# Optimization experiments

Hardware: AMD Instinct MI355X
Metric: run time of the kernel (lower is better)

The kernel has to match this reference:

```python
import jax, jax.numpy as jnp
import numpy as np

WINDOW = 256   # init kwarg window_size
CAUSAL = False # init kwarg causal


def setup_inputs() -> dict:
    key = jax.random.key(0)
    k1, k2, k3 = jax.random.split(key, 3)
    shape = (2, 16, 4096, 64)  # (batch, heads, seq_len, head_dim); seq_len % WINDOW == 0
    return {
        "query": jax.random.normal(k1, shape, dtype=jnp.float32),
        "key": jax.random.normal(k2, shape, dtype=jnp.float32),
        "value": jax.random.normal(k3, shape, dtype=jnp.float32),
    }


def _neighbor_blocks(x, nb, W):
    # x: [B,H,S,D] -> [B,H,nb,3W,D] where block n holds key blocks n-1,n,n+1 (zero padded at ends)
    B, H, S, D = x.shape
    xb = x.reshape(B, H, nb, W, D)
    xp = jnp.pad(xb, ((0, 0), (0, 0), (1, 1), (0, 0), (0, 0)))
    return jnp.concatenate([xp[:, :, j:j + nb] for j in range(3)], axis=3)


def _swa(query, key, value, window, causal):
    B, H, S, D = query.shape
    W = window
    nb = S // W
    scale = jnp.float32(1.0 / np.sqrt(D))
    qb = query.reshape(B, H, nb, W, D)
    kb = _neighbor_blocks(key, nb, W)    # [B,H,nb,3W,D]
    vb = _neighbor_blocks(value, nb, W)  # [B,H,nb,3W,D]

    # band mask: query global pos qi = n*W + q, key global pos ki = n*W + (k - W)
    qpos = jnp.arange(W)[:, None]              # [W,1]
    kpos = jnp.arange(3 * W)[None, :] - W      # [1,3W] relative block offset
    diff = kpos - qpos                         # [W,3W] == ki - qi
    ki = jnp.arange(nb)[:, None, None] * W + kpos[None]  # [nb,1,3W]
    valid = (ki >= 0) & (ki < S)
    if causal:
        band = (diff >= -W) & (diff <= 0)
    else:
        band = jnp.abs(diff) <= W
    mask = valid & band[None]                  # [nb,W,3W]

    scores = jnp.einsum('bhnqd,bhnkd->bhnqk', qb, kb) * scale  # [B,H,nb,W,3W]
    scores = jnp.where(mask, scores, -jnp.inf)
    attn = jax.nn.softmax(scores, axis=-1)
    out = jnp.einsum('bhnqk,bhnkd->bhnqd', attn, vb)
    return out.reshape(B, H, S, D)


def reference(query, key, value):
    return _swa(query, key, value, WINDOW, CAUSAL)
```

## Files before the change

### kernel.cpp

```cpp
#include <hip/hip_runtime.h>
#include <hip/hip_bf16.h>

typedef __attribute__((ext_vector_type(4)))  float f32x4;
typedef __attribute__((ext_vector_type(16))) float f32x16;
typedef __attribute__((ext_vector_type(8)))  short bf16x8;
typedef __attribute__((ext_vector_type(4)))  unsigned u32x4;

#define S_LEN 4096
#define HEAD_D 64
#define WIN 256
#define QBLK 128
#define KVBLK 64
#define KSTR 72
#define VSTR 72
#define QSCALE 0.18033688f

#define KBYTES (KVBLK * KSTR * 2)
#define VBYTES (HEAD_D * VSTR * 2)
#define KHALF  (KBYTES / 2)
#define VHALF  (VBYTES / 2)
#define LPAR_OFF (2 * KBYTES + 2 * VBYTES)
#define SMEM_BYTES (LPAR_OFF + 2 * 4 * 32 * 4)

static __device__ __forceinline__ unsigned cvt2(float lo, float hi) {
  unsigned r;
  asm("v_cvt_pk_bf16_f32 %0, %1, %2" : "=v"(r) : "v"(lo), "v"(hi));
  return r;
}

#define PUB_BARRIER() do {                              \
    __builtin_amdgcn_sched_barrier(0);                  \
    asm volatile("s_waitcnt lgkmcnt(0)" ::: "memory");  \
    __builtin_amdgcn_s_barrier();                       \
    __builtin_amdgcn_sched_barrier(0);                  \
  } while (0)

__global__ __launch_bounds__(512, 4)
void swa_fwd(const float* __restrict__ Q, const float* __restrict__ K,
             const float* __restrict__ V, float* __restrict__ O) {
  __shared__ __attribute__((aligned(16))) char smem[SMEM_BYTES];

  const int tid  = threadIdx.x;
  const int widx = tid >> 6;
  const int lane = tid & 63;
  const int hi   = lane >> 5;
  const int c    = lane & 31;
  const int qg   = widx & 3;
  const int kh   = widx >> 2;
  const int kho  = kh * 32;

  const int pb  = blockIdx.x;
  const int bh  = (pb & 7) * 4 + ((pb >> 3) >> 5);
  const int qb  = (pb >> 3) & 31;
  const int bq0 = qb * QBLK;
  const int q0w = bq0 + qg * 32;

  const size_t base = (size_t)bh * S_LEN * HEAD_D;
  const float* Qp = Q + base;
  const float* Kp = K + base;
  const float* Vp = V + base;
  float*       Op = O + base;

  const f32x16 Z16 = {0.f,0.f,0.f,0.f,0.f,0.f,0.f,0.f,0.f,0.f,0.f,0.f,0.f,0.f,0.f,0.f};

  bf16x8 aq[4];
  {
    const float* qr = Qp + (size_t)(q0w + c) * HEAD_D + hi * 8;
    #pragma unroll
    for (int ch = 0; ch < 4; ++ch) {
      f32x4 x0 = *(const f32x4*)(qr + ch * 16);
      f32x4 x1 = *(const f32x4*)(qr + ch * 16 + 4);
      u32x4 au;
      au[0] = cvt2(x0[0] * QSCALE, x0[1] * QSCALE);
      au[1] = cvt2(x0[2] * QSCALE, x0[3] * QSCALE);
      au[2] = cvt2(x1[0] * QSCALE, x1[1] * QSCALE);
      au[3] = cvt2(x1[2] * QSCALE, x1[3] * QSCALE);
      aq[ch] = __builtin_bit_cast(bf16x8, au);
    }
  }

  f32x16 acc0 = Z16, acc1 = Z16;
  float lsA = 0.f, lsB = 0.f;

  const int lo   = max(0, bq0 - WIN);
  const int khiB = min(S_LEN, bq0 + QBLK + WIN);
  const int nt   = (khiB - lo) >> 6;

  const int krow  = tid >> 3;
  const int kc8   = (tid & 7) << 3;
  const int key2  = (tid & 31) << 1;
  const int key2p = (key2 & ~12) | ((key2 & 4) << 1) | ((key2 & 8) >> 1);
  const int vd4   = (tid >> 5) << 2;

  short* const ksh = (short*)smem;
  short* const vsh = (short*)(smem + 2 * KBYTES);
  const short* const krd = ksh + (kho + c) * KSTR + hi * 8;
  const short* const vrd = vsh + c * VSTR + kho + hi * 8;
  short* const kwr = ksh + krow * KSTR + kc8;
  short* const vwr = vsh + vd4 * VSTR + key2p;

  unsigned koff = (unsigned)(lo + krow) * HEAD_D + kc8;
  unsigned voff = (unsigned)(lo + key2) * HEAD_D + vd4;

  f32x4 ka0, ka1, va0, va1;
  #define LOAD_TILE() do {                          \
    ka0 = *(const f32x4*)(Kp + koff);               \
    ka1 = *(const f32x4*)(Kp + koff + 4);           \
    va0 = *(const f32x4*)(Vp + voff);               \
    va1 = *(const f32x4*)(Vp + voff + HEAD_D);      \
    koff += KVBLK * HEAD_D;                         \
    voff += KVBLK * HEAD_D;                         \
  } while (0)

  #define STAGE_TO(BUF) do {                                        \
    u32x4 kw;                                                       \
    kw[0] = cvt2(ka0[0], ka0[1]);                                   \
    kw[1] = cvt2(ka0[2], ka0[3]);                                   \
    kw[2] = cvt2(ka1[0], ka1[1]);                                   \
    kw[3] = cvt2(ka1[2], ka1[3]);                                   \
    *(u32x4*)&kwr[(BUF) * KHALF] = kw;                              \
    _Pragma("unroll")                                               \
    for (int j = 0; j < 4; ++j)                                     \
      *(unsigned*)&vwr[(BUF) * VHALF + j * VSTR] = cvt2(va0[j], va1[j]); \
  } while (0)

  #define TILE_BODY(T, BUF) do {                                              \
    const int kv0_ = lo + ((T) << 6);                                         \
    f32x16 s = Z16;                                                           \
    __builtin_amdgcn_s_setprio(1);                                            \
    _Pragma("unroll")                                                         \
    for (int ch = 0; ch < 4; ++ch) {                                          \
      bf16x8 akf = *(const bf16x8*)&krd[(BUF) * KHALF + ch * 16];             \
      s = __builtin_amdgcn_mfma_f32_32x32x16_bf16(akf, aq[ch], s, 0, 0, 0);   \
    }                                                                         \
    __builtin_amdgcn_s_setprio(0);                                            \
    if ((T) + 1 < nt) {                                                       \
      STAGE_TO((BUF) ^ 1);                                                    \
      if ((T) + 2 < nt) LOAD_TILE();                                          \
    }                                                                         \
    const int rel_ = kv0_ + kho - q0w;                                        \
    if (rel_ >= -224 && rel_ <= 224) {                                        \
      _Pragma("unroll")                                                       \
      for (int g = 0; g < 16; g += 2) {                                       \
        const float p0 = __builtin_amdgcn_exp2f(s[g]);                        \
        const float p1 = __builtin_amdgcn_exp2f(s[g + 1]);                    \
        s[g] = p0; s[g + 1] = p1; lsA += p0; lsB += p1;                       \
      }                                                                       \
    } else {                                                                  \
      const int bm_ = rel_ + 4 * hi - c + WIN;                                \
      _Pragma("unroll")                                                       \
      for (int g = 0; g < 16; ++g) {                                          \
        const int ro_ = (g & 3) + 8 * (g >> 2);                               \
        const float p = ((unsigned)(bm_ + ro_) <= 2u * WIN)                   \
                          ? __builtin_amdgcn_exp2f(s[g]) : 0.f;               \
        s[g] = p; if (g & 1) lsB += p; else lsA += p;                         \
      }                                                                       \
    }                                                                         \
    __builtin_amdgcn_s_setprio(1);                                            \
    _Pragma("unroll")                                                         \
    for (int kt = 0; kt < 2; ++kt) {                                          \
      u32x4 pau;                                                              \
      _Pragma("unroll")                                                       \
      for (int p2 = 0; p2 < 4; ++p2)                                          \
        pau[p2] = cvt2(s[kt * 8 + 2 * p2], s[kt * 8 + 2 * p2 + 1]);           \
      const bf16x8 pa = __builtin_bit_cast(bf16x8, pau);                      \
      bf16x8 bv0 = *(const bf16x8*)&vrd[(BUF) * VHALF + kt * 16];             \
      acc0 = __builtin_amdgcn_mfma_f32_32x32x16_bf16(pa, bv0, acc0, 0, 0, 0); \
      bf16x8 bv1 = *(const bf16x8*)&vrd[(BUF) * VHALF + kt * 16 + 32 * VSTR]; \
      acc1 = __builtin_amdgcn_mfma_f32_32x32x16_bf16(pa, bv1, acc1, 0, 0, 0); \
    }                                                                         \
    __builtin_amdgcn_s_setprio(0);                                            \
    if ((T) + 1 < nt) PUB_BARRIER();                                          \
  } while (0)

  LOAD_TILE();
  STAGE_TO(0);
  LOAD_TILE();
  PUB_BARRIER();

  for (int t = 0; t < nt; t += 2) {
    TILE_BODY(t, 0);
    TILE_BODY(t + 1, 1);
  }

  float lsum = lsA + lsB;
  lsum += __shfl_xor(lsum, 32);
  __syncthreads();
  float* o_mrg = (float*)smem;
  float* l_par = (float*)(smem + LPAR_OFF);
  if (hi == 0) l_par[(kh * 4 + qg) * 32 + c] = lsum;
  if (kh == 0) {
    #pragma unroll
    for (int g = 0; g < 16; ++g) {
      const int qrow = (g & 3) + 8 * (g >> 2) + 4 * hi;
      o_mrg[(qg * 32 + qrow) * HEAD_D + c]      = acc0[g];
      o_mrg[(qg * 32 + qrow) * HEAD_D + 32 + c] = acc1[g];
    }
  }
  __syncthreads();
  if (kh == 1) {
    if (hi == 0) l_par[qg * 32 + c] = 1.0f / (l_par[qg * 32 + c] + l_par[(4 + qg) * 32 + c]);
    __asm__ volatile("s_waitcnt lgkmcnt(0)" ::: "memory");
    __builtin_amdgcn_sched_barrier(0);
    #pragma unroll
    for (int g = 0; g < 16; ++g) {
      const int qrow = (g & 3) + 8 * (g >> 2) + 4 * hi;
      const float iv = l_par[qg * 32 + qrow];
      float* orow = Op + (size_t)(q0w + qrow) * HEAD_D;
      orow[c]      = (o_mrg[(qg * 32 + qrow) * HEAD_D + c]      + acc0[g]) * iv;
      orow[32 + c] = (o_mrg[(qg * 32 + qrow) * HEAD_D + 32 + c] + acc1[g]) * iv;
    }
  }
}

extern "C" void kernel_launch(void* const* d_in, const int* in_sizes, int n_in,
                              void* d_out, int out_size, void* d_ws, size_t ws_size,
                              hipStream_t stream) {
  const float* q = (const float*)d_in[0];
  const float* k = (const float*)d_in[1];
  const float* v = (const float*)d_in[2];
  float* o = (float*)d_out;
  const int blocks = 2 * 16 * (S_LEN / QBLK);
  swa_fwd<<<dim3(blocks), dim3(512), 0, stream>>>(q, k, v, o);
}
```

Baseline: 47.22 us.

## Process KV tiles in pairs with four-buffer LDS and one barrier per pair

Restructures the main loop so each period computes QK^T for two 64-key tiles at once, from four LDS buffers (two pairs, ping-ponged). This halves the barriers and interleaves two independent MFMA chains. Staging of the next pair is spread between the softmax/PV phases. LDS use doubles (now dynamic shared memory with a per-launch attribute call) and launch bounds drop to 2 blocks per CU, which cuts occupancy and raises register pressure from holding two score tiles.

```diff
diff --git a/kernel.cpp b/kernel.cpp
--- a/kernel.cpp
+++ b/kernel.cpp
@@ -16,11 +16,10 @@
 #define QSCALE 0.18033688f
 
 #define KBYTES (KVBLK * KSTR * 2)
-#define VBYTES (HEAD_D * VSTR * 2)
-#define KHALF  (KBYTES / 2)
-#define VHALF  (VBYTES / 2)
-#define LPAR_OFF (2 * KBYTES + 2 * VBYTES)
-#define SMEM_BYTES (LPAR_OFF + 2 * 4 * 32 * 4)
+#define KELEM  (KVBLK * KSTR)
+#define VELEM  (HEAD_D * VSTR)
+#define LPAR_OFF (8 * KBYTES)
+#define SMEM_TOTAL (LPAR_OFF + 2 * 4 * 32 * 4)
 
 static __device__ __forceinline__ unsigned cvt2(float lo, float hi) {
   unsigned r;
@@ -35,10 +34,10 @@
     __builtin_amdgcn_sched_barrier(0);                  \
   } while (0)
 
-__global__ __launch_bounds__(512, 4)
+__global__ __launch_bounds__(512, 2)
 void swa_fwd(const float* __restrict__ Q, const float* __restrict__ K,
              const float* __restrict__ V, float* __restrict__ O) {
-  __shared__ __attribute__((aligned(16))) char smem[SMEM_BYTES];
+  extern __shared__ __align__(16) char smem[];
 
   const int tid  = threadIdx.x;
   const int widx = tid >> 6;
@@ -85,6 +84,7 @@
   const int lo   = max(0, bq0 - WIN);
   const int khiB = min(S_LEN, bq0 + QBLK + WIN);
   const int nt   = (khiB - lo) >> 6;
+  const int np   = nt >> 1;
 
   const int krow  = tid >> 3;
   const int kc8   = (tid & 7) << 3;
@@ -93,7 +93,7 @@
   const int vd4   = (tid >> 5) << 2;
 
   short* const ksh = (short*)smem;
-  short* const vsh = (short*)(smem + 2 * KBYTES);
+  short* const vsh = (short*)(smem + 4 * KBYTES);
   const short* const krd = ksh + (kho + c) * KSTR + hi * 8;
   const short* const vrd = vsh + c * VSTR + kho + hi * 8;
   short* const kwr = ksh + krow * KSTR + kc8;
@@ -118,69 +118,86 @@
     kw[1] = cvt2(ka0[2], ka0[3]);                                   \
     kw[2] = cvt2(ka1[0], ka1[1]);                                   \
     kw[3] = cvt2(ka1[2], ka1[3]);                                   \
-    *(u32x4*)&kwr[(BUF) * KHALF] = kw;                              \
+    *(u32x4*)&kwr[(BUF) * KELEM] = kw;                              \
     _Pragma("unroll")                                               \
     for (int j = 0; j < 4; ++j)                                     \
-      *(unsigned*)&vwr[(BUF) * VHALF + j * VSTR] = cvt2(va0[j], va1[j]); \
-  } while (0)
-
-  #define TILE_BODY(T, BUF) do {                                              \
-    const int kv0_ = lo + ((T) << 6);                                         \
-    f32x16 s = Z16;                                                           \
-    __builtin_amdgcn_s_setprio(1);                                            \
-    _Pragma("unroll")                                                         \
-    for (int ch = 0; ch < 4; ++ch) {                                          \
-      bf16x8 akf = *(const bf16x8*)&krd[(BUF) * KHALF + ch * 16];             \
-      s = __builtin_amdgcn_mfma_f32_32x32x16_bf16(akf, aq[ch], s, 0, 0, 0);   \
-    }                                                                         \
-    __builtin_amdgcn_s_setprio(0);                                            \
-    if ((T) + 1 < nt) {                                                       \
-      STAGE_TO((BUF) ^ 1);                                                    \
-      if ((T) + 2 < nt) LOAD_TILE();                                          \
-    }                                                                         \
-    const int rel_ = kv0_ + kho - q0w;                                        \
-    if (rel_ >= -224 && rel_ <= 224) {                                        \
+      *(unsigned*)&vwr[(BUF) * VELEM + j * VSTR] = cvt2(va0[j], va1[j]); \
+  } while (0)
+
+  #define SOFTMAX(SV, REL) do {                                               \
+    if ((REL) >= -224 && (REL) <= 224) {                                      \
       _Pragma("unroll")                                                       \
       for (int g = 0; g < 16; g += 2) {                                       \
-        const float p0 = __builtin_amdgcn_exp2f(s[g]);                        \
-        const float p1 = __builtin_amdgcn_exp2f(s[g + 1]);                    \
-        s[g] = p0; s[g + 1] = p1; lsA += p0; lsB += p1;                       \
+        const float p0 = __builtin_amdgcn_exp2f((SV)[g]);                     \
+        const float p1 = __builtin_amdgcn_exp2f((SV)[g + 1]);                 \
+        (SV)[g] = p0; (SV)[g + 1] = p1; lsA += p0; lsB += p1;                 \
       }                                                                       \
     } else {                                                                  \
-      const int bm_ = rel_ + 4 * hi - c + WIN;                                \
+      const int bm_ = (REL) + 4 * hi - c + WIN;                               \
       _Pragma("unroll")                                                       \
       for (int g = 0; g < 16; ++g) {                                          \
         const int ro_ = (g & 3) + 8 * (g >> 2);                               \
         const float p = ((unsigned)(bm_ + ro_) <= 2u * WIN)                   \
-                          ? __builtin_amdgcn_exp2f(s[g]) : 0.f;               \
-        s[g] = p; if (g & 1) lsB += p; else lsA += p;                         \
+                          ? __builtin_amdgcn_exp2f((SV)[g]) : 0.f;            \
+        (SV)[g] = p; if (g & 1) lsB += p; else lsA += p;                      \
       }                                                                       \
     }                                                                         \
+  } while (0)
+
+  #define PV(SV, BUF) do {                                                    \
     __builtin_amdgcn_s_setprio(1);                                            \
     _Pragma("unroll")                                                         \
     for (int kt = 0; kt < 2; ++kt) {                                          \
       u32x4 pau;                                                              \
       _Pragma("unroll")                                                       \
       for (int p2 = 0; p2 < 4; ++p2)                                          \
-        pau[p2] = cvt2(s[kt * 8 + 2 * p2], s[kt * 8 + 2 * p2 + 1]);           \
+        pau[p2] = cvt2((SV)[kt * 8 + 2 * p2], (SV)[kt * 8 + 2 * p2 + 1]);     \
       const bf16x8 pa = __builtin_bit_cast(bf16x8, pau);                      \
-      bf16x8 bv0 = *(const bf16x8*)&vrd[(BUF) * VHALF + kt * 16];             \
+      bf16x8 bv0 = *(const bf16x8*)&vrd[(BUF) * VELEM + kt * 16];             \
       acc0 = __builtin_amdgcn_mfma_f32_32x32x16_bf16(pa, bv0, acc0, 0, 0, 0); \
-      bf16x8 bv1 = *(const bf16x8*)&vrd[(BUF) * VHALF + kt * 16 + 32 * VSTR]; \
+      bf16x8 bv1 = *(const bf16x8*)&vrd[(BUF) * VELEM + kt * 16 + 32 * VSTR]; \
       acc1 = __builtin_amdgcn_mfma_f32_32x32x16_bf16(pa, bv1, acc1, 0, 0, 0); \
     }                                                                         \
     __builtin_amdgcn_s_setprio(0);                                            \
-    if ((T) + 1 < nt) PUB_BARRIER();                                          \
+  } while (0)
+
+  #define PERIOD(PP, PAIR) do {                                               \
+    const int BA = 2 * (PAIR), BB = BA + 1;                                   \
+    const int TGA = 2 * ((PAIR) ^ 1), TGB = TGA + 1;                          \
+    const bool more_ = (PP) + 1 < np;                                         \
+    const int rel_a = lo + ((PP) << 7) + kho - q0w;                           \
+    if (more_) LOAD_TILE();                 \
+    f32x16 s_a = Z16, s_b = Z16;                                              \
+    __builtin_amdgcn_s_setprio(1);             \
+    _Pragma("unroll")                                                         \
+    for (int ch = 0; ch < 4; ++ch) {                                          \
+      bf16x8 akfA = *(const bf16x8*)&krd[BA * KELEM + ch * 16];               \
+      s_a = __builtin_amdgcn_mfma_f32_32x32x16_bf16(akfA, aq[ch], s_a, 0,0,0);\
+      bf16x8 akfB = *(const bf16x8*)&krd[BB * KELEM + ch * 16];               \
+      s_b = __builtin_amdgcn_mfma_f32_32x32x16_bf16(akfB, aq[ch], s_b, 0,0,0);\
+    }                                                                         \
+    __builtin_amdgcn_s_setprio(0);                                            \
+    if (more_) {                                                              \
+      STAGE_TO(TGA);                            \
+      LOAD_TILE();                       \
+    }                                                                         \
+    SOFTMAX(s_a, rel_a);                                                      \
+    PV(s_a, BA);                                                              \
+    if (more_) STAGE_TO(TGB);                                                 \
+    SOFTMAX(s_b, rel_a + 64);                                                 \
+    PV(s_b, BB);                                                              \
+    if (more_) PUB_BARRIER();                                                 \
   } while (0)
 
   LOAD_TILE();
   STAGE_TO(0);
   LOAD_TILE();
+  STAGE_TO(1);
   PUB_BARRIER();
 
-  for (int t = 0; t < nt; t += 2) {
-    TILE_BODY(t, 0);
-    TILE_BODY(t + 1, 1);
+  for (int pp = 0; pp < np; pp += 2) {
+    PERIOD(pp, 0);
+    if (pp + 1 < np) PERIOD(pp + 1, 1);
   }
 
   float lsum = lsA + lsB;
@@ -220,6 +237,10 @@
   const float* k = (const float*)d_in[1];
   const float* v = (const float*)d_in[2];
   float* o = (float*)d_out;
+  static int attr_done = 0;
+  hipFuncSetAttribute((const void*)swa_fwd,
+                      hipFuncAttributeMaxDynamicSharedMemorySize, SMEM_TOTAL);
+  (void)attr_done;
   const int blocks = 2 * 16 * (S_LEN / QBLK);
-  swa_fwd<<<dim3(blocks), dim3(512), 0, stream>>>(q, k, v, o);
+  swa_fwd<<<dim3(blocks), dim3(512), SMEM_TOTAL, stream>>>(q, k, v, o);
 }
```

Measured after the change: 56.22 us. 19.0% more time.
